# Performance work log

Hardware: AMD Instinct MI355X
Metric: run time of the kernel (lower is better)

## Reference

```python
import jax, jax.numpy as jnp
import numpy as np

NUM_HEADS = 8
EPS = 1e-6


def _edge_boost(x, density_weight):
    # x: [B, C, H, W] -> boost: [B, H*W] (per-query additive bias)
    B, C, H, W = x.shape
    sx = jnp.array([[-1., 0., 1.], [-2., 0., 2.], [-1., 0., 1.]], dtype=x.dtype)
    sy = jnp.array([[-1., -2., -1.], [0., 0., 0.], [1., 2., 1.]], dtype=x.dtype)
    feat_mean = x.mean(axis=1, keepdims=True)            # [B,1,H,W]
    kern = jnp.stack([sx, sy])[:, None]                  # [2,1,3,3] (OIHW)
    g = jax.lax.conv_general_dilated(
        feat_mean, kern, window_strides=(1, 1), padding='SAME',
        dimension_numbers=('NCHW', 'OIHW', 'NCHW'))     # [B,2,H,W]
    edge = jnp.sqrt(g[:, 0] ** 2 + g[:, 1] ** 2 + EPS)   # [B,H,W]
    return density_weight * jnp.log1p(edge.reshape(B, H * W))


def setup_inputs() -> dict:
    key = jax.random.key(0)
    k1, k2, k3 = jax.random.split(key, 3)
    B, C, H, W = 2, 256, 56, 56
    x = jax.random.normal(k1, (B, C, H, W), dtype=jnp.float32)
    Wqkv = jax.random.normal(k2, (3 * C, C), dtype=jnp.float32) * 0.02
    Wproj = jax.random.normal(k3, (C, C), dtype=jnp.float32) * 0.02
    bproj = jnp.zeros((C,), dtype=jnp.float32)
    density_weight = jnp.float32(1.0)
    return {"x": x, "Wqkv": Wqkv, "Wproj": Wproj, "bproj": bproj,
            "density_weight": density_weight}


def reference(x, Wqkv, Wproj, bproj, density_weight):
    B, C, H, W = x.shape
    h = NUM_HEADS
    d = C // h
    N = H * W
    scale = d ** -0.5

    x_flat = x.reshape(B, C, N).transpose(0, 2, 1)        # [B,N,C]
    qkv = x_flat @ Wqkv.T                                 # [B,N,3C]
    qkv = qkv.reshape(B, N, 3, h, d).transpose(2, 0, 3, 1, 4)  # [3,B,h,N,d]
    q, k, v = qkv[0], qkv[1], qkv[2]

    attn = jnp.einsum('bhqd,bhkd->bhqk', q, k) * scale    # [B,h,N,N]
    boost = _edge_boost(x, density_weight)                # [B,N]
    attn = attn + boost[:, None, :, None]                 # per-query bias, bcast over heads/keys
    attn = jax.nn.softmax(attn, axis=-1)
    # dropout is identity in eval mode

    out = jnp.einsum('bhqk,bhkd->bhqd', attn, v)          # [B,h,N,d]
    out = out.transpose(0, 2, 1, 3).reshape(B, N, C)      # [B,N,C]
    out = out @ Wproj.T + bproj
    return out.transpose(0, 2, 1).reshape(B, C, H, W)
```

## Files before the change

### kernel.cpp

```cpp
#include <hip/hip_runtime.h>
#include <hip/hip_bf16.h>
#include <math.h>

#define NQ    3136
#define CDIM  256
#define HEADS 8
#define NT    49


typedef __attribute__((ext_vector_type(8))) short short8;
typedef __attribute__((ext_vector_type(4))) float f32x4;

__device__ __forceinline__ short f2bf(float f) {
    union { float f; unsigned u; } v; v.f = f;
    unsigned r = v.u + 0x7fff + ((v.u >> 16) & 1);
    return (short)(r >> 16);
}

__device__ __forceinline__ unsigned pk_bf16(float a, float b) {
    unsigned r;
    asm("v_cvt_pk_bf16_f32 %0, %1, %2" : "=v"(r) : "v"(a), "v"(b));
    return r;
}

#define SCALE_L2E 0.25503487523f

__global__ __launch_bounds__(256) void prep(const float* __restrict__ x,
                                            const float* __restrict__ Wq,
                                            const float* __restrict__ Wp,
                                            short* __restrict__ xT,
                                            short* __restrict__ Wb,
                                            short* __restrict__ Wpb) {
    const int bx = blockIdx.x;
    const int t  = threadIdx.x;
    if (bx == 52) {
        const int wp   = blockIdx.y + 4 * blockIdx.z;
        const int base = wp * 8192 + t * 4;
        #pragma unroll
        for (int i = 0; i < 8; ++i) {
            float4 v = *(const float4*)(Wp + base + i * 1024);
            uint2 o = { pk_bf16(v.x, v.y), pk_bf16(v.z, v.w) };
            *(uint2*)(Wpb + base + i * 1024) = o;
        }
        return;
    }
    if (bx >= 49) {
        const int wb   = (bx - 49) + 3 * (blockIdx.y + 4 * blockIdx.z);
        const int base = wb * 8192 + t * 4;
        #pragma unroll
        for (int i = 0; i < 8; ++i) {
            float4 v = *(const float4*)(Wq + base + i * 1024);
            uint2 o = { pk_bf16(v.x, v.y), pk_bf16(v.z, v.w) };
            *(uint2*)(Wb + base + i * 1024) = o;
        }
        return;
    }
    __shared__ short lt[64][72];
    const int b = blockIdx.z, cb = blockIdx.y, nb = bx;
    const float* xb = x + (size_t)b * CDIM * NQ + (size_t)(cb * 64) * NQ + nb * 64;
    #pragma unroll
    for (int it = 0; it < 4; ++it) {
        const int cc = (t >> 4) + 16 * it;
        const int nn = (t & 15) * 4;
        float4 v = *(const float4*)(xb + (size_t)cc * NQ + nn);
        lt[nn + 0][cc] = f2bf(v.x);
        lt[nn + 1][cc] = f2bf(v.y);
        lt[nn + 2][cc] = f2bf(v.z);
        lt[nn + 3][cc] = f2bf(v.w);
    }
    __syncthreads();
    const int n2 = t >> 2, c2 = (t & 3) * 16;
    short* dst = xT + ((size_t)b * NQ + nb * 64 + n2) * CDIM + cb * 64 + c2;
    *(uint4*)dst       = *(const uint4*)&lt[n2][c2];
    *(uint4*)(dst + 8) = *(const uint4*)&lt[n2][c2 + 8];
}

__global__ __launch_bounds__(256) void qkv_mfma(const short* __restrict__ xT,
                                                const short* __restrict__ Wb,
                                                short* __restrict__ Qs,
                                                short* __restrict__ Kb,
                                                short* __restrict__ Vt) {
    __shared__ short xs[64][40];
    __shared__ short wsm[64][40];
    __shared__ short eps[64][72];
    const int nb = blockIdx.x, jb = blockIdx.y, b = blockIdx.z;
    const int n0 = nb * 64, j0 = jb * 64;
    const int t = threadIdx.x;
    const int lane = t & 63, w = t >> 6, g = lane >> 4, ql = lane & 15;
    const int srow = t >> 2, sc = (t & 3) * 8;

    const short* xsrc = xT + ((size_t)b * NQ + n0 + srow) * CDIM + sc;
    const short* wsrc = Wb + (size_t)(j0 + srow) * CDIM + sc;

    short8 xr = *(const short8*)(xsrc);
    short8 wr = *(const short8*)(wsrc);

    f32x4 acc[4] = {};
    for (int c0 = 0; c0 < 256; c0 += 32) {
        *(short8*)&xs[srow][sc]  = xr;
        *(short8*)&wsm[srow][sc] = wr;
        __syncthreads();
        if (c0 + 32 < 256) {
            xr = *(const short8*)(xsrc + c0 + 32);
            wr = *(const short8*)(wsrc + c0 + 32);
        }
        short8 bf = *(const short8*)&wsm[16 * w + ql][8 * g];
        #pragma unroll
        for (int r = 0; r < 4; ++r) {
            short8 af = *(const short8*)&xs[16 * r + ql][8 * g];
            acc[r] = __builtin_amdgcn_mfma_f32_16x16x32_bf16(af, bf, acc[r], 0, 0, 0);
        }
        __syncthreads();
    }

    const int sect = jb >> 2;
    const int hb   = (jb & 3) * 2;
    const int jloc = 16 * w + ql;

    if (sect < 2) {
        const float sc2 = (sect == 0) ? SCALE_L2E : 1.0f;
        #pragma unroll
        for (int r = 0; r < 4; ++r)
            #pragma unroll
            for (int i = 0; i < 4; ++i)
                eps[16 * r + 4 * g + i][jloc] = f2bf(acc[r][i] * sc2);
        __syncthreads();
        short* dstb = (sect == 0) ? Qs : Kb;
        const int n2 = t >> 2, jc = (t & 3) * 16;
        const int head = hb + (jc >> 5), d0 = jc & 31;
        short* dst = dstb + ((size_t)(b * 8 + head) * NQ + n0 + n2) * 32 + d0;
        *(uint4*)dst       = *(const uint4*)&eps[n2][jc];
        *(uint4*)(dst + 8) = *(const uint4*)&eps[n2][jc + 8];
    } else {
        #pragma unroll
        for (int r = 0; r < 4; ++r)
            #pragma unroll
            for (int i = 0; i < 4; ++i)
                eps[jloc][16 * r + 4 * g + i] = f2bf(acc[r][i]);
        __syncthreads();
        const int jl = t >> 2, nc = (t & 3) * 16;
        short* dst = Vt + ((size_t)(b * 8 + hb + (jl >> 5)) * 32 + (jl & 31)) * NQ + n0 + nc;
        *(uint4*)dst       = *(const uint4*)&eps[jl][nc];
        *(uint4*)(dst + 8) = *(const uint4*)&eps[jl][nc + 8];
    }
}

__global__ __launch_bounds__(256) void attn_mfma(const short* __restrict__ Qs,
                                                 const short* __restrict__ Kb,
                                                 const short* __restrict__ Vt,
                                                 short* __restrict__ Ob) {
    __shared__ __align__(16) short vts[2][2][32][72];
    __shared__ __align__(16) short pq[4][32][72];

    const int bid = blockIdx.x;
    const int xcd = bid & 7;
    const int ii  = bid >> 3;
    const int bh  = xcd * 2 + (ii & 1);
    const int q0  = (ii >> 1) * 64;

    const int t    = threadIdx.x;
    const int lane = t & 63;
    const int w    = t >> 6;
    const int g    = lane >> 4;
    const int ql   = lane & 15;
    const int qg   = w & 1, half = w >> 1;
    const int qbase = q0 + 32 * qg;

    const short* Qh = Qs + (size_t)bh * NQ * 32;
    const short* Kh = Kb + (size_t)bh * NQ * 32;
    const short* Vh = Vt + (size_t)bh * 32 * NQ;

    const short8 qfA = *(const short8*)(Qh + (size_t)(qbase + ql) * 32 + 8 * g);
    const short8 qfB = *(const short8*)(Qh + (size_t)(qbase + 16 + ql) * 32 + 8 * g);

    short8 ones;
    #pragma unroll
    for (int e = 0; e < 8; ++e) ones[e] = (short)0x3F80;

    const short* kp = Kh + (size_t)ql * 32 + 8 * g;

    const int vrow = (t & 127) >> 2;
    const int vu   = (t & 3) * 16;

    f32x4 otA0 = {0,0,0,0}, otA1 = {0,0,0,0};
    f32x4 otB0 = {0,0,0,0}, otB1 = {0,0,0,0};
    f32x4 otlA = {0,0,0,0}, otlB = {0,0,0,0};

    short8 vr0 = *(const short8*)(Vh + (size_t)vrow * NQ + half * 64 + vu);
    short8 vr1 = *(const short8*)(Vh + (size_t)vrow * NQ + half * 64 + vu + 8);
    *(short8*)&vts[half][0][vrow][vu]     = vr0;
    *(short8*)&vts[half][0][vrow][vu + 8] = vr1;
    __syncthreads();

    int buf = 0;
    for (int i = 0; i < 25; ++i) {
        const int cur = 2 * i + half;
        const int nxt = cur + 2;
        if (nxt < NT) {
            vr0 = *(const short8*)(Vh + (size_t)vrow * NQ + nxt * 64 + vu);
            vr1 = *(const short8*)(Vh + (size_t)vrow * NQ + nxt * 64 + vu + 8);
        }

        if (cur < NT) {
            const int k0 = cur * 64;
            short8 kf0 = *(const short8*)(kp + (size_t)(k0 +  0) * 32);
            short8 kf1 = *(const short8*)(kp + (size_t)(k0 + 16) * 32);
            short8 kf2 = *(const short8*)(kp + (size_t)(k0 + 32) * 32);
            short8 kf3 = *(const short8*)(kp + (size_t)(k0 + 48) * 32);

            __builtin_amdgcn_s_setprio(1);
            f32x4 stA[4], stB[4];
            stA[0] = __builtin_amdgcn_mfma_f32_16x16x32_bf16(kf0, qfA, (f32x4){0,0,0,0}, 0, 0, 0);
            stB[0] = __builtin_amdgcn_mfma_f32_16x16x32_bf16(kf0, qfB, (f32x4){0,0,0,0}, 0, 0, 0);
            stA[1] = __builtin_amdgcn_mfma_f32_16x16x32_bf16(kf1, qfA, (f32x4){0,0,0,0}, 0, 0, 0);
            stB[1] = __builtin_amdgcn_mfma_f32_16x16x32_bf16(kf1, qfB, (f32x4){0,0,0,0}, 0, 0, 0);
            stA[2] = __builtin_amdgcn_mfma_f32_16x16x32_bf16(kf2, qfA, (f32x4){0,0,0,0}, 0, 0, 0);
            stB[2] = __builtin_amdgcn_mfma_f32_16x16x32_bf16(kf2, qfB, (f32x4){0,0,0,0}, 0, 0, 0);
            stA[3] = __builtin_amdgcn_mfma_f32_16x16x32_bf16(kf3, qfA, (f32x4){0,0,0,0}, 0, 0, 0);
            stB[3] = __builtin_amdgcn_mfma_f32_16x16x32_bf16(kf3, qfB, (f32x4){0,0,0,0}, 0, 0, 0);
            __builtin_amdgcn_s_setprio(0);

            float pA[16], pB[16];
            #pragma unroll
            for (int c = 0; c < 4; ++c)
                #pragma unroll
                for (int e = 0; e < 4; ++e) {
                    pA[4 * c + e] = __builtin_amdgcn_exp2f(stA[c][e]);
                    pB[4 * c + e] = __builtin_amdgcn_exp2f(stB[c][e]);
                }

            #pragma unroll
            for (int c = 0; c < 4; ++c) {
                uint2 va_ = { pk_bf16(pA[4 * c + 0], pA[4 * c + 1]),
                              pk_bf16(pA[4 * c + 2], pA[4 * c + 3]) };
                *(uint2*)&pq[w][ql][16 * c + 4 * g] = va_;
                uint2 vb_ = { pk_bf16(pB[4 * c + 0], pB[4 * c + 1]),
                              pk_bf16(pB[4 * c + 2], pB[4 * c + 3]) };
                *(uint2*)&pq[w][16 + ql][16 * c + 4 * g] = vb_;
            }
            asm volatile("s_waitcnt lgkmcnt(0)" ::: "memory");

            short8 pbA0 = *(const short8*)&pq[w][ql][8 * g];
            short8 pbA1 = *(const short8*)&pq[w][ql][32 + 8 * g];
            short8 pbB0 = *(const short8*)&pq[w][16 + ql][8 * g];
            short8 pbB1 = *(const short8*)&pq[w][16 + ql][32 + 8 * g];
            short8 va00 = *(const short8*)&vts[half][buf][ql][8 * g];
            short8 va01 = *(const short8*)&vts[half][buf][ql][32 + 8 * g];
            short8 va10 = *(const short8*)&vts[half][buf][16 + ql][8 * g];
            short8 va11 = *(const short8*)&vts[half][buf][16 + ql][32 + 8 * g];

            __builtin_amdgcn_s_setprio(1);
            otA0 = __builtin_amdgcn_mfma_f32_16x16x32_bf16(va00, pbA0, otA0, 0, 0, 0);
            otA0 = __builtin_amdgcn_mfma_f32_16x16x32_bf16(va01, pbA1, otA0, 0, 0, 0);
            otA1 = __builtin_amdgcn_mfma_f32_16x16x32_bf16(va10, pbA0, otA1, 0, 0, 0);
            otA1 = __builtin_amdgcn_mfma_f32_16x16x32_bf16(va11, pbA1, otA1, 0, 0, 0);
            otB0 = __builtin_amdgcn_mfma_f32_16x16x32_bf16(va00, pbB0, otB0, 0, 0, 0);
            otB0 = __builtin_amdgcn_mfma_f32_16x16x32_bf16(va01, pbB1, otB0, 0, 0, 0);
            otB1 = __builtin_amdgcn_mfma_f32_16x16x32_bf16(va10, pbB0, otB1, 0, 0, 0);
            otB1 = __builtin_amdgcn_mfma_f32_16x16x32_bf16(va11, pbB1, otB1, 0, 0, 0);
            otlA = __builtin_amdgcn_mfma_f32_16x16x32_bf16(ones, pbA0, otlA, 0, 0, 0);
            otlA = __builtin_amdgcn_mfma_f32_16x16x32_bf16(ones, pbA1, otlA, 0, 0, 0);
            otlB = __builtin_amdgcn_mfma_f32_16x16x32_bf16(ones, pbB0, otlB, 0, 0, 0);
            otlB = __builtin_amdgcn_mfma_f32_16x16x32_bf16(ones, pbB1, otlB, 0, 0, 0);
            __builtin_amdgcn_s_setprio(0);
        }

        if (nxt < NT) {
            *(short8*)&vts[half][buf ^ 1][vrow][vu]     = vr0;
            *(short8*)&vts[half][buf ^ 1][vrow][vu + 8] = vr1;
        }
        __syncthreads();
        buf ^= 1;
    }

    const float lA = otlA[0];
    const float lB = otlB[0];

    float* mrg = (float*)&pq[0][0][0];
    if (half == 1) {
        float* pp = mrg + ((size_t)qg * 64 + lane) * 20;
        *(f32x4*)(pp + 0)  = otA0;
        *(f32x4*)(pp + 4)  = otA1;
        *(f32x4*)(pp + 8)  = otB0;
        *(f32x4*)(pp + 12) = otB1;
        pp[16] = lA; pp[17] = lB;
    }
    __syncthreads();
    if (half == 0) {
        const float* pp = mrg + ((size_t)qg * 64 + lane) * 20;
        f32x4 a0 = *(const f32x4*)(pp + 0);
        f32x4 a1 = *(const f32x4*)(pp + 4);
        f32x4 b0 = *(const f32x4*)(pp + 8);
        f32x4 b1 = *(const f32x4*)(pp + 12);
        const float invA = 1.f / (lA + pp[16]);
        const float invB = 1.f / (lB + pp[17]);
        const int b = bh >> 3, h = bh & 7;
        short* orowA = Ob + ((size_t)b * NQ + qbase + ql) * CDIM + h * 32;
        short* orowB = Ob + ((size_t)b * NQ + qbase + 16 + ql) * CDIM + h * 32;
        uint2 wA0 = { pk_bf16((otA0[0]+a0[0])*invA, (otA0[1]+a0[1])*invA),
                      pk_bf16((otA0[2]+a0[2])*invA, (otA0[3]+a0[3])*invA) };
        uint2 wA1 = { pk_bf16((otA1[0]+a1[0])*invA, (otA1[1]+a1[1])*invA),
                      pk_bf16((otA1[2]+a1[2])*invA, (otA1[3]+a1[3])*invA) };
        uint2 wB0 = { pk_bf16((otB0[0]+b0[0])*invB, (otB0[1]+b0[1])*invB),
                      pk_bf16((otB0[2]+b0[2])*invB, (otB0[3]+b0[3])*invB) };
        uint2 wB1 = { pk_bf16((otB1[0]+b1[0])*invB, (otB1[1]+b1[1])*invB),
                      pk_bf16((otB1[2]+b1[2])*invB, (otB1[3]+b1[3])*invB) };
        *(uint2*)(orowA + 4 * g)      = wA0;
        *(uint2*)(orowA + 16 + 4 * g) = wA1;
        *(uint2*)(orowB + 4 * g)      = wB0;
        *(uint2*)(orowB + 16 + 4 * g) = wB1;
    }
}

__global__ __launch_bounds__(256) void proj_mfma(const short* __restrict__ Ob,
                                                 const short* __restrict__ Wpb,
                                                 const float* __restrict__ bias,
                                                 float* __restrict__ out) {
    __shared__ short xs[32][40];
    __shared__ short wsm[64][40];
    __shared__ float eps[64][36];
    const int n0  = blockIdx.x * 32;
    const int co0 = blockIdx.y * 64;
    const int b   = blockIdx.z;
    const int t   = threadIdx.x;
    const int lane = t & 63, w = t >> 6, g = lane >> 4, ql = lane & 15;
    const int arow = (t & 127) >> 2, ac = (t & 3) * 8;
    const int brow = t >> 2,          bc = (t & 3) * 8;

    const short* asrc = Ob + ((size_t)b * NQ + n0 + arow) * CDIM + ac;
    const short* wsrc = Wpb + (size_t)(co0 + brow) * CDIM + bc;

    short8 ar = {};
    if (t < 128) ar = *(const short8*)(asrc);
    short8 wr = *(const short8*)(wsrc);

    f32x4 acc0 = {}, acc1 = {};
    for (int c0 = 0; c0 < 256; c0 += 32) {
        if (t < 128) *(short8*)&xs[arow][ac] = ar;
        *(short8*)&wsm[brow][bc] = wr;
        __syncthreads();
        if (c0 + 32 < 256) {
            if (t < 128) ar = *(const short8*)(asrc + c0 + 32);
            wr = *(const short8*)(wsrc + c0 + 32);
        }
        short8 bfr = *(const short8*)&wsm[16 * w + ql][8 * g];
        short8 af0 = *(const short8*)&xs[ql][8 * g];
        short8 af1 = *(const short8*)&xs[16 + ql][8 * g];
        acc0 = __builtin_amdgcn_mfma_f32_16x16x32_bf16(af0, bfr, acc0, 0, 0, 0);
        acc1 = __builtin_amdgcn_mfma_f32_16x16x32_bf16(af1, bfr, acc1, 0, 0, 0);
        __syncthreads();
    }

    const int jl = 16 * w + ql;
    const float bb = bias[co0 + jl];
    *(float4*)&eps[jl][4 * g]      = make_float4(acc0[0] + bb, acc0[1] + bb,
                                                 acc0[2] + bb, acc0[3] + bb);
    *(float4*)&eps[jl][16 + 4 * g] = make_float4(acc1[0] + bb, acc1[1] + bb,
                                                 acc1[2] + bb, acc1[3] + bb);
    __syncthreads();

    const int row = t >> 2, seg = (t & 3) * 8;
    float* outp = out + ((size_t)b * CDIM + co0 + row) * NQ + n0 + seg;
    *(float4*)(outp)     = *(const float4*)&eps[row][seg];
    *(float4*)(outp + 4) = *(const float4*)&eps[row][seg + 4];
}

extern "C" void kernel_launch(void* const* d_in, const int* in_sizes, int n_in,
                              void* d_out, int out_size, void* d_ws, size_t ws_size,
                              hipStream_t stream) {
    const float* x     = (const float*)d_in[0];
    const float* Wqkv  = (const float*)d_in[1];
    const float* Wproj = (const float*)d_in[2];
    const float* bproj = (const float*)d_in[3];
    float* out = (float*)d_out;

    short* xT  = (short*)d_ws;
    short* Wb  = xT + (size_t)2 * NQ * CDIM;
    short* Wpb = Wb + (size_t)768 * CDIM;
    short* Qs  = Wpb + (size_t)CDIM * CDIM;
    short* Kb  = Qs + (size_t)16 * NQ * 32;
    short* Vt  = Kb + (size_t)16 * NQ * 32;
    short* Ob  = Vt + (size_t)16 * NQ * 32;

    prep<<<dim3(53, 4, 2), 256, 0, stream>>>(x, Wqkv, Wproj, xT, Wb, Wpb);
    qkv_mfma<<<dim3(49, 12, 2), 256, 0, stream>>>(xT, Wb, Qs, Kb, Vt);
    attn_mfma<<<dim3(784, 1, 1), 256, 0, stream>>>(Qs, Kb, Vt, Ob);
    proj_mfma<<<dim3(98, 4, 2), 256, 0, stream>>>(Ob, Wpb, bproj, out);
}
```

Measured before the change: 69.40 us.

## Store V in MFMA fragment order and load it directly into registers

The QKV kernel now writes V in a tiled layout that already matches the MFMA A-operand fragment order. Each lane of the attention kernel can then load its V fragments straight from global memory into registers. This removes the shared-memory V staging buffer, its double buffering, and the per-iteration __syncthreads. It also cuts LDS usage, which may raise occupancy. The cost is that V comes from global or L2 through per-lane 16-byte loads issued every iteration, with prefetch held in registers rather than LDS.

```diff
diff --git a/kernel.cpp b/kernel.cpp
--- a/kernel.cpp
+++ b/kernel.cpp
@@ -79,7 +79,7 @@
                                                 const short* __restrict__ Wb,
                                                 short* __restrict__ Qs,
                                                 short* __restrict__ Kb,
-                                                short* __restrict__ Vt) {
+                                                short* __restrict__ V4) {
     __shared__ short xs[64][40];
     __shared__ short wsm[64][40];
     __shared__ short eps[64][72];
@@ -138,18 +138,24 @@
             for (int i = 0; i < 4; ++i)
                 eps[jloc][16 * r + 4 * g + i] = f2bf(acc[r][i]);
         __syncthreads();
-        const int jl = t >> 2, nc = (t & 3) * 16;
-        short* dst = Vt + ((size_t)(b * 8 + hb + (jl >> 5)) * 32 + (jl & 31)) * NQ + n0 + nc;
-        *(uint4*)dst       = *(const uint4*)&eps[jl][nc];
-        *(uint4*)(dst + 8) = *(const uint4*)&eps[jl][nc + 8];
+        const int f  = t >> 6;
+        const int l2 = t & 63;
+        const int gg = l2 >> 4, qq = l2 & 15;
+        const int dl = ((f & 2) ? 16 : 0) + qq;
+        const int ko = ((f & 1) ? 32 : 0) + 8 * gg;
+        #pragma unroll
+        for (int h2 = 0; h2 < 2; ++h2) {
+            const uint4 val = *(const uint4*)&eps[32 * h2 + dl][ko];
+            short* dst = V4 + ((((size_t)(b * 8 + hb + h2) * NT + nb) * 4 + f) * 64 + l2) * 8;
+            *(uint4*)dst = val;
+        }
     }
 }
 
 __global__ __launch_bounds__(256) void attn_mfma(const short* __restrict__ Qs,
                                                  const short* __restrict__ Kb,
-                                                 const short* __restrict__ Vt,
+                                                 const short* __restrict__ V4,
                                                  short* __restrict__ Ob) {
-    __shared__ __align__(16) short vts[2][2][32][72];
     __shared__ __align__(16) short pq[4][32][72];
 
     const int bid = blockIdx.x;
@@ -168,7 +174,7 @@
 
     const short* Qh = Qs + (size_t)bh * NQ * 32;
     const short* Kh = Kb + (size_t)bh * NQ * 32;
-    const short* Vh = Vt + (size_t)bh * 32 * NQ;
+    const short* Vh = V4 + (size_t)bh * (NT * 2048) + (size_t)lane * 8;
 
     const short8 qfA = *(const short8*)(Qh + (size_t)(qbase + ql) * 32 + 8 * g);
     const short8 qfB = *(const short8*)(Qh + (size_t)(qbase + 16 + ql) * 32 + 8 * g);
@@ -179,27 +185,25 @@
 
     const short* kp = Kh + (size_t)ql * 32 + 8 * g;
 
-    const int vrow = (t & 127) >> 2;
-    const int vu   = (t & 3) * 16;
-
     f32x4 otA0 = {0,0,0,0}, otA1 = {0,0,0,0};
     f32x4 otB0 = {0,0,0,0}, otB1 = {0,0,0,0};
     f32x4 otlA = {0,0,0,0}, otlB = {0,0,0,0};
 
-    short8 vr0 = *(const short8*)(Vh + (size_t)vrow * NQ + half * 64 + vu);
-    short8 vr1 = *(const short8*)(Vh + (size_t)vrow * NQ + half * 64 + vu + 8);
-    *(short8*)&vts[half][0][vrow][vu]     = vr0;
-    *(short8*)&vts[half][0][vrow][vu + 8] = vr1;
-    __syncthreads();
-
-    int buf = 0;
+    const short* vt0 = Vh + half * 2048;
+    short8 vc00 = *(const short8*)(vt0);
+    short8 vc01 = *(const short8*)(vt0 + 512);
+    short8 vc10 = *(const short8*)(vt0 + 1024);
+    short8 vc11 = *(const short8*)(vt0 + 1536);
+
     for (int i = 0; i < 25; ++i) {
         const int cur = 2 * i + half;
         const int nxt = cur + 2;
-        if (nxt < NT) {
-            vr0 = *(const short8*)(Vh + (size_t)vrow * NQ + nxt * 64 + vu);
-            vr1 = *(const short8*)(Vh + (size_t)vrow * NQ + nxt * 64 + vu + 8);
-        }
+        const int tn  = (nxt < NT) ? nxt : 48;
+        const short* vtn = Vh + (size_t)tn * 2048;
+        short8 vn00 = *(const short8*)(vtn);
+        short8 vn01 = *(const short8*)(vtn + 512);
+        short8 vn10 = *(const short8*)(vtn + 1024);
+        short8 vn11 = *(const short8*)(vtn + 1536);
 
         if (cur < NT) {
             const int k0 = cur * 64;
@@ -244,20 +248,16 @@
             short8 pbA1 = *(const short8*)&pq[w][ql][32 + 8 * g];
             short8 pbB0 = *(const short8*)&pq[w][16 + ql][8 * g];
             short8 pbB1 = *(const short8*)&pq[w][16 + ql][32 + 8 * g];
-            short8 va00 = *(const short8*)&vts[half][buf][ql][8 * g];
-            short8 va01 = *(const short8*)&vts[half][buf][ql][32 + 8 * g];
-            short8 va10 = *(const short8*)&vts[half][buf][16 + ql][8 * g];
-            short8 va11 = *(const short8*)&vts[half][buf][16 + ql][32 + 8 * g];
 
             __builtin_amdgcn_s_setprio(1);
-            otA0 = __builtin_amdgcn_mfma_f32_16x16x32_bf16(va00, pbA0, otA0, 0, 0, 0);
-            otA0 = __builtin_amdgcn_mfma_f32_16x16x32_bf16(va01, pbA1, otA0, 0, 0, 0);
-            otA1 = __builtin_amdgcn_mfma_f32_16x16x32_bf16(va10, pbA0, otA1, 0, 0, 0);
-            otA1 = __builtin_amdgcn_mfma_f32_16x16x32_bf16(va11, pbA1, otA1, 0, 0, 0);
-            otB0 = __builtin_amdgcn_mfma_f32_16x16x32_bf16(va00, pbB0, otB0, 0, 0, 0);
-            otB0 = __builtin_amdgcn_mfma_f32_16x16x32_bf16(va01, pbB1, otB0, 0, 0, 0);
-            otB1 = __builtin_amdgcn_mfma_f32_16x16x32_bf16(va10, pbB0, otB1, 0, 0, 0);
-            otB1 = __builtin_amdgcn_mfma_f32_16x16x32_bf16(va11, pbB1, otB1, 0, 0, 0);
+            otA0 = __builtin_amdgcn_mfma_f32_16x16x32_bf16(vc00, pbA0, otA0, 0, 0, 0);
+            otA0 = __builtin_amdgcn_mfma_f32_16x16x32_bf16(vc01, pbA1, otA0, 0, 0, 0);
+            otA1 = __builtin_amdgcn_mfma_f32_16x16x32_bf16(vc10, pbA0, otA1, 0, 0, 0);
+            otA1 = __builtin_amdgcn_mfma_f32_16x16x32_bf16(vc11, pbA1, otA1, 0, 0, 0);
+            otB0 = __builtin_amdgcn_mfma_f32_16x16x32_bf16(vc00, pbB0, otB0, 0, 0, 0);
+            otB0 = __builtin_amdgcn_mfma_f32_16x16x32_bf16(vc01, pbB1, otB0, 0, 0, 0);
+            otB1 = __builtin_amdgcn_mfma_f32_16x16x32_bf16(vc10, pbB0, otB1, 0, 0, 0);
+            otB1 = __builtin_amdgcn_mfma_f32_16x16x32_bf16(vc11, pbB1, otB1, 0, 0, 0);
             otlA = __builtin_amdgcn_mfma_f32_16x16x32_bf16(ones, pbA0, otlA, 0, 0, 0);
             otlA = __builtin_amdgcn_mfma_f32_16x16x32_bf16(ones, pbA1, otlA, 0, 0, 0);
             otlB = __builtin_amdgcn_mfma_f32_16x16x32_bf16(ones, pbB0, otlB, 0, 0, 0);
@@ -265,17 +265,13 @@
             __builtin_amdgcn_s_setprio(0);
         }
 
-        if (nxt < NT) {
-            *(short8*)&vts[half][buf ^ 1][vrow][vu]     = vr0;
-            *(short8*)&vts[half][buf ^ 1][vrow][vu + 8] = vr1;
-        }
-        __syncthreads();
-        buf ^= 1;
+        vc00 = vn00; vc01 = vn01; vc10 = vn10; vc11 = vn11;
     }
 
     const float lA = otlA[0];
     const float lB = otlB[0];
 
+    __syncthreads();
     float* mrg = (float*)&pq[0][0][0];
     if (half == 1) {
         float* pp = mrg + ((size_t)qg * 64 + lane) * 20;
@@ -379,11 +375,11 @@
     short* Wpb = Wb + (size_t)768 * CDIM;
     short* Qs  = Wpb + (size_t)CDIM * CDIM;
     short* Kb  = Qs + (size_t)16 * NQ * 32;
-    short* Vt  = Kb + (size_t)16 * NQ * 32;
-    short* Ob  = Vt + (size_t)16 * NQ * 32;
+    short* V4  = Kb + (size_t)16 * NQ * 32;
+    short* Ob  = V4 + (size_t)16 * NT * 2048;
 
     prep<<<dim3(53, 4, 2), 256, 0, stream>>>(x, Wqkv, Wproj, xT, Wb, Wpb);
-    qkv_mfma<<<dim3(49, 12, 2), 256, 0, stream>>>(xT, Wb, Qs, Kb, Vt);
-    attn_mfma<<<dim3(784, 1, 1), 256, 0, stream>>>(Qs, Kb, Vt, Ob);
+    qkv_mfma<<<dim3(49, 12, 2), 256, 0, stream>>>(xT, Wb, Qs, Kb, V4);
+    attn_mfma<<<dim3(784, 1, 1), 256, 0, stream>>>(Qs, Kb, V4, Ob);
     proj_mfma<<<dim3(98, 4, 2), 256, 0, stream>>>(Ob, Wpb, bproj, out);
 }
```

Result: slower. 70.89 us (+2.1%).
